# Optimization experiments

Measured on AMD Instinct MI355X. Metric: run time of the kernel, lower is better.

The kernel has to match this reference:

```python
import jax, jax.numpy as jnp
import numpy as np

B, C, D, H, W = 4, 64, 32, 64, 64
S, NH = 8, 4
HD = C // NH


def setup_inputs() -> dict:
    key = jax.random.key(0)
    ks = jax.random.split(key, 8)
    sc = 0.05
    return {
        "x": jax.random.normal(ks[0], (B, C, D, H, W), jnp.float32),
        "slot_init": jax.random.normal(ks[1], (1, C, S), jnp.float32),
        "slot_proj_w": jax.random.normal(ks[2], (C, C), jnp.float32) * sc,
        "slot_proj_b": jnp.zeros((C,), jnp.float32),
        "ln_g": jnp.ones((C,), jnp.float32),
        "ln_b": jnp.zeros((C,), jnp.float32),
        "in_proj_w": jax.random.normal(ks[3], (3 * C, C), jnp.float32) * sc,
        "in_proj_b": jnp.zeros((3 * C,), jnp.float32),
        "out_proj_w": jax.random.normal(ks[4], (C, C), jnp.float32) * sc,
        "out_proj_b": jnp.zeros((C,), jnp.float32),
        "feat_w": jax.random.normal(ks[5], (C, C), jnp.float32) * sc,
        "feat_b": jnp.zeros((C,), jnp.float32),
        "s2f_w": jax.random.normal(ks[6], (C, C), jnp.float32) * sc,
        "s2f_b": jnp.zeros((C,), jnp.float32),
    }


def _l2norm(v, axis):
    # F.normalize: v / max(||v||, eps)
    n = jnp.sqrt(jnp.sum(v * v, axis=axis, keepdims=True))
    return v / jnp.maximum(n, 1e-12)


def reference(x, slot_init, slot_proj_w, slot_proj_b, ln_g, ln_b,
              in_proj_w, in_proj_b, out_proj_w, out_proj_b,
              feat_w, feat_b, s2f_w, s2f_b):
    b, c, d, h, w = x.shape
    n = d * h * w
    x_flat = x.reshape(b, c, n)                                  # (b,c,N)
    slots = jnp.broadcast_to(slot_init, (b, c, S))               # (b,c,S)

    # ---- slot update: cosine-sim cross attention over N ----
    x_norm = _l2norm(x_flat, 1)
    slots_norm = _l2norm(slots, 1)
    sim = jnp.einsum('bcs,bcn->bsn', slots_norm, x_norm)         # (b,S,N)
    attn = jax.nn.softmax(sim, axis=2)
    updates = jnp.einsum('bcn,bsn->bsc', x_flat, attn)           # (b,S,c)
    slots_t = updates @ slot_proj_w.T + slot_proj_b              # (b,S,c)

    # ---- LayerNorm(channels) then tiny MHSA over S=8 slots ----
    mu = jnp.mean(slots_t, axis=-1, keepdims=True)
    var = jnp.mean((slots_t - mu) ** 2, axis=-1, keepdims=True)
    sn = (slots_t - mu) / jnp.sqrt(var + 1e-5) * ln_g + ln_b     # (b,S,c)

    qkv = sn @ in_proj_w.T + in_proj_b                           # (b,S,3c)
    q, k, v = jnp.split(qkv, 3, axis=-1)
    def heads(t):
        return t.reshape(b, S, NH, HD).transpose(0, 2, 1, 3)     # (b,H,S,hd)
    q, k, v = heads(q), heads(k), heads(v)
    scores = jnp.einsum('bhqd,bhkd->bhqk', q, k) / jnp.sqrt(jnp.float32(HD))
    a = jax.nn.softmax(scores, axis=-1)
    o = jnp.einsum('bhqk,bhkd->bhqd', a, v).transpose(0, 2, 1, 3).reshape(b, S, c)
    o = o @ out_proj_w.T + out_proj_b
    slots_t = slots_t + o                                        # (b,S,c)

    # ---- feature broadcast: 1x1x1 conv + slot->feature attention ----
    feat_flat = jnp.einsum('oc,bcn->bon', feat_w, x_flat) + feat_b[None, :, None]
    slots_feat = slots_t @ s2f_w.T + s2f_b                       # (b,S,c)
    sim2 = jnp.einsum('bsc,bcn->bsn', slots_feat, feat_flat)
    attn2 = jax.nn.softmax(sim2, axis=1)                         # softmax over slots
    out = jnp.einsum('bsc,bsn->bcn', slots_t, attn2)             # (b,c,N)
    return out.reshape(b, c, d, h, w) + x
```

## Files before the change

### kernel.cpp

```cpp
#include <hip/hip_runtime.h>
#include <hip/hip_bf16.h>

#define BB   4
#define CC   64
#define SS   8
#define NN   (32*64*64)
#define NH_  4
#define HD_  16
#define TN   256

typedef __attribute__((ext_vector_type(8))) short bf16x8;
typedef __attribute__((ext_vector_type(4))) float f32x4;

__device__ __forceinline__ float b2f(unsigned short h) {
    union { unsigned u; float f; } v; v.u = ((unsigned)h) << 16; return v.f;
}
__device__ __forceinline__ unsigned short f2b(float f) {
    union { float f; unsigned u; } v; v.f = f;
    unsigned r = v.u + 0x7FFFu + ((v.u >> 16) & 1u);
    return (unsigned short)(r >> 16);
}
__device__ __forceinline__ unsigned bfpack(float a, float b) {
    union { float f; unsigned u; } x, y; x.f = a; y.f = b;
    unsigned ra = (x.u + 0x7FFFu + ((x.u >> 16) & 1u)) >> 16;
    unsigned rb = (y.u + 0x7FFFu + ((y.u >> 16) & 1u)) & 0xFFFF0000u;
    return ra | rb;
}

__global__ __launch_bounds__(256) void k_slots_attn(
    const float* __restrict__ x, const float* __restrict__ slot_init,
    float* __restrict__ U_part, float* __restrict__ sume_part, int bpb)
{
    __shared__ short xt[CC * TN];
    __shared__ short et[16 * TN];
    __shared__ float snT[SS * CC];
    __shared__ float snorm[SS];
    __shared__ float red[SS * 256];

    const int tid = threadIdx.x;
    const int b   = blockIdx.x / bpb;
    const int blk = blockIdx.x % bpb;

    *(int4*)&et[8*TN + tid*8] = make_int4(0, 0, 0, 0);

    if (tid < SS) {
        float ss = 0.f;
        for (int c = 0; c < CC; ++c) { float v = slot_init[c*SS + tid]; ss += v*v; }
        snorm[tid] = fmaxf(sqrtf(ss), 1e-12f);
    }
    __syncthreads();
    if (tid < CC) {
        for (int s = 0; s < SS; ++s) snT[s*CC + tid] = slot_init[tid*SS + s] / snorm[s];
    }
    __syncthreads();

    const int lane = tid & 63, wv = tid >> 6;
    const int cS = tid >> 2, nq = tid & 3;
    f32x4 accU = {0.f, 0.f, 0.f, 0.f};
    float accS[SS];
    #pragma unroll
    for (int s = 0; s < SS; ++s) accS[s] = 0.f;

    const float* xb = x + (size_t)b * CC * NN;
    const int ntiles = NN / TN;

    for (int t = blk; t < ntiles; t += bpb) {
        const int n0 = t * TN;

        {
            const float* srcrow = xb + (size_t)cS * NN + n0;
            #pragma unroll
            for (int i = 0; i < 8; ++i) {
                const int n = nq*8 + i*32;
                float4 va = *(const float4*)(srcrow + n);
                float4 vb = *(const float4*)(srcrow + n + 4);
                int4 o;
                o.x = (int)bfpack(va.x, va.y);
                o.y = (int)bfpack(va.z, va.w);
                o.z = (int)bfpack(vb.x, vb.y);
                o.w = (int)bfpack(vb.z, vb.w);
                const int slot = (nq + i*4) ^ (cS & 7);
                *(int4*)&xt[cS*TN + (slot << 3)] = o;
            }
        }
        __syncthreads();

        {
            const int nq3 = tid >> 3, n7 = tid & 7;
            float ss = 0.f;
            float a[SS];
            #pragma unroll
            for (int s = 0; s < SS; ++s) a[s] = 0.f;
            #pragma unroll
            for (int c4 = 0; c4 < 16; ++c4) {
                float xv[4];
                #pragma unroll
                for (int j = 0; j < 4; ++j) {
                    const int c = c4*4 + j;
                    unsigned short h = (unsigned short)xt[c*TN + (((nq3 ^ (c & 7)) << 3) | n7)];
                    xv[j] = b2f(h);
                    ss += xv[j] * xv[j];
                }
                #pragma unroll
                for (int s = 0; s < SS; ++s) {
                    const float4 g4 = *(const float4*)&snT[s*CC + c4*4];
                    a[s] += g4.x*xv[0] + g4.y*xv[1] + g4.z*xv[2] + g4.w*xv[3];
                }
            }
            const float invn = 1.f / fmaxf(sqrtf(ss), 1e-12f);
            #pragma unroll
            for (int s = 0; s < SS; ++s) {
                float e = __expf(a[s] * invn);
                accS[s] += e;
                et[s*TN + (((nq3 ^ s) << 3) | n7)] = (short)f2b(e);
            }
        }
        __syncthreads();

        {
            const int ca = (wv << 4) + (lane & 15);
            const int rb = lane & 15;
            const int p  = lane >> 4;
            #pragma unroll
            for (int k = 0; k < TN/32; ++k) {
                const int sa = ((((k << 2) + p) ^ (lane & 7)) << 3);
                bf16x8 af = *(const bf16x8*)&xt[ca*TN + sa];
                bf16x8 bfr = *(const bf16x8*)&et[rb*TN + sa];
                accU = __builtin_amdgcn_mfma_f32_16x16x32_bf16(af, bfr, accU, 0, 0, 0);
            }
        }
        __syncthreads();
    }

    {
        const size_t base = ((size_t)(b*bpb + blk) * SS) * CC;
        if ((lane & 15) < SS) {
            const int s  = lane & 15;
            const int c0 = (wv << 4) + ((lane >> 4) << 2);
            #pragma unroll
            for (int r = 0; r < 4; ++r)
                U_part[base + s*CC + c0 + r] = accU[r];
        }
    }
    #pragma unroll
    for (int s = 0; s < SS; ++s) red[s*256 + tid] = accS[s];
    __syncthreads();
    {
        const int s = tid >> 5, j = tid & 31;
        float v = 0.f;
        #pragma unroll
        for (int k = 0; k < 8; ++k) v += red[s*256 + j*8 + k];
        v += __shfl_xor(v, 1); v += __shfl_xor(v, 2); v += __shfl_xor(v, 4);
        v += __shfl_xor(v, 8); v += __shfl_xor(v, 16);
        if (j == 0) sume_part[(size_t)(b*bpb + blk)*SS + s] = v;
    }
}

__global__ __launch_bounds__(256) void k_precomp(
    const float* __restrict__ s2fw, const float* __restrict__ s2fb,
    const float* __restrict__ fw, const float* __restrict__ fb,
    float* __restrict__ M, float* __restrict__ g0v,
    float* __restrict__ hv, float* __restrict__ h0)
{
    const int tid = threadIdx.x;
    if (blockIdx.x < 16) {
        const int cp = blockIdx.x*4 + (tid >> 6);
        const int c  = tid & 63;
        float acc = 0.f;
        #pragma unroll 8
        for (int o = 0; o < CC; ++o)
            acc += s2fw[o*CC + cp] * fw[o*CC + c];
        M[cp*CC + c] = acc;
    } else {
        if (tid < 64) {
            float acc = 0.f;
            #pragma unroll 8
            for (int o = 0; o < CC; ++o) acc += s2fb[o] * fw[o*CC + tid];
            g0v[tid] = acc;
        } else if (tid < 128) {
            const int cp = tid - 64;
            float acc = 0.f;
            #pragma unroll 8
            for (int o = 0; o < CC; ++o) acc += s2fw[o*CC + cp] * fb[o];
            hv[cp] = acc;
        } else if (tid == 128) {
            float acc = 0.f;
            for (int o = 0; o < CC; ++o) acc += s2fb[o] * fb[o];
            *h0 = acc;
        }
    }
}

__global__ __launch_bounds__(256) void k_reduce2(
    const float* __restrict__ U_part, const float* __restrict__ sume_part,
    float* __restrict__ upd_g, int bpb)
{
    __shared__ float part[4][64];
    __shared__ float lbuf[256];
    __shared__ float Lsh;
    const int tid = threadIdx.x;
    const int b = blockIdx.x >> 3, s = blockIdx.x & 7;
    const int c = tid & 63, kc = tid >> 6;
    const int cnt = bpb >> 2;

    lbuf[tid] = (tid < bpb) ? sume_part[(size_t)(b*bpb + tid)*SS + s] : 0.f;

    float acc = 0.f;
    const float* base = U_part + ((size_t)(b*bpb + kc*cnt)*SS + s)*CC + c;
    for (int k = 0; k < cnt; ++k)
        acc += base[(size_t)k * SS * CC];
    part[kc][c] = acc;
    __syncthreads();

    if (tid < 128) lbuf[tid] += lbuf[tid + 128];
    __syncthreads();
    if (tid < 64) {
        float v = lbuf[tid] + lbuf[tid + 64];
        v += __shfl_xor(v, 1); v += __shfl_xor(v, 2); v += __shfl_xor(v, 4);
        v += __shfl_xor(v, 8); v += __shfl_xor(v, 16); v += __shfl_xor(v, 32);
        if (tid == 0) Lsh = v;
    }
    __syncthreads();

    if (tid < 64) {
        float u = part[0][c] + part[1][c] + part[2][c] + part[3][c];
        upd_g[((size_t)b*SS + s)*CC + c] = u / Lsh;
    }
}

__global__ __launch_bounds__(256) void k_slots_small(
    const float* __restrict__ upd_g,
    const float* __restrict__ spw, const float* __restrict__ spb,
    const float* __restrict__ lng, const float* __restrict__ lnb,
    const float* __restrict__ ipw, const float* __restrict__ ipb,
    const float* __restrict__ opw, const float* __restrict__ opb,
    const float* __restrict__ M, const float* __restrict__ g0v,
    const float* __restrict__ hv, const float* __restrict__ h0,
    float* __restrict__ st_out, float* __restrict__ g_out, float* __restrict__ h_out)
{
    __shared__ float upd[SS*CC];
    __shared__ float st [SS*CC];
    __shared__ float snb[SS*CC];
    __shared__ float qkv[SS*3*CC];
    __shared__ float ot [SS*CC];

    const int tid  = threadIdx.x;
    const int b    = blockIdx.x;
    const int c    = tid & 63;
    const int quad = tid >> 6;
    const int r0 = quad*2, r1 = r0 + 1;
    float wreg[CC];

    #pragma unroll
    for (int i = 0; i < 16; ++i)
        *(float4*)&wreg[i*4] = *(const float4*)(spw + c*CC + i*4);
    upd[r0*CC + c] = upd_g[(b*SS + r0)*CC + c];
    upd[r1*CC + c] = upd_g[(b*SS + r1)*CC + c];
    __syncthreads();

    {
        const float bias = spb[c];
        float a0 = bias, a1 = bias;
        #pragma unroll
        for (int i = 0; i < 16; ++i) {
            float4 u0 = *(const float4*)&upd[r0*CC + i*4];
            float4 u1 = *(const float4*)&upd[r1*CC + i*4];
            a0 += u0.x*wreg[i*4+0] + u0.y*wreg[i*4+1] + u0.z*wreg[i*4+2] + u0.w*wreg[i*4+3];
            a1 += u1.x*wreg[i*4+0] + u1.y*wreg[i*4+1] + u1.z*wreg[i*4+2] + u1.w*wreg[i*4+3];
        }
        st[r0*CC + c] = a0;
        st[r1*CC + c] = a1;
    }
    __syncthreads();

    {
        const int row = tid >> 5, l = tid & 31;
        float v0 = st[row*CC + l], v1 = st[row*CC + l + 32];
        float sum = v0 + v1;
        sum += __shfl_xor(sum, 1); sum += __shfl_xor(sum, 2); sum += __shfl_xor(sum, 4);
        sum += __shfl_xor(sum, 8); sum += __shfl_xor(sum, 16);
        const float mu = sum * (1.f/64.f);
        const float d0 = v0 - mu, d1 = v1 - mu;
        float vs = d0*d0 + d1*d1;
        vs += __shfl_xor(vs, 1); vs += __shfl_xor(vs, 2); vs += __shfl_xor(vs, 4);
        vs += __shfl_xor(vs, 8); vs += __shfl_xor(vs, 16);
        const float rstd = rsqrtf(vs * (1.f/64.f) + 1e-5f);
        snb[row*CC + l]      = d0 * rstd * lng[l]      + lnb[l];
        snb[row*CC + l + 32] = d1 * rstd * lng[l + 32] + lnb[l + 32];
    }
    __syncthreads();

    for (int m = 0; m < 3; ++m) {
        #pragma unroll
        for (int i = 0; i < 16; ++i)
            *(float4*)&wreg[i*4] = *(const float4*)(ipw + (size_t)(m*CC + c)*CC + i*4);
        const float bias = ipb[m*CC + c];
        float a0 = bias, a1 = bias;
        #pragma unroll
        for (int i = 0; i < 16; ++i) {
            float4 u0 = *(const float4*)&snb[r0*CC + i*4];
            float4 u1 = *(const float4*)&snb[r1*CC + i*4];
            a0 += u0.x*wreg[i*4+0] + u0.y*wreg[i*4+1] + u0.z*wreg[i*4+2] + u0.w*wreg[i*4+3];
            a1 += u1.x*wreg[i*4+0] + u1.y*wreg[i*4+1] + u1.z*wreg[i*4+2] + u1.w*wreg[i*4+3];
        }
        qkv[r0*3*CC + m*CC + c] = a0;
        qkv[r1*3*CC + m*CC + c] = a1;
    }
    __syncthreads();

    if (tid < NH_*SS) {
        const int h = tid >> 3, q = tid & 7;
        float qreg[HD_];
        #pragma unroll
        for (int i = 0; i < 4; ++i)
            *(float4*)&qreg[i*4] = *(const float4*)&qkv[q*3*CC + h*HD_ + i*4];
        float srow[SS];
        float mx = -1e30f;
        #pragma unroll
        for (int k = 0; k < SS; ++k) {
            float acc = 0.f;
            #pragma unroll
            for (int d = 0; d < HD_; ++d)
                acc += qreg[d] * qkv[k*3*CC + CC + h*HD_ + d];
            srow[k] = acc * 0.25f;
            mx = fmaxf(mx, srow[k]);
        }
        float l = 0.f;
        #pragma unroll
        for (int k = 0; k < SS; ++k) { srow[k] = __expf(srow[k] - mx); l += srow[k]; }
        const float inv = 1.f / l;
        float oreg[HD_];
        #pragma unroll
        for (int d = 0; d < HD_; ++d) oreg[d] = 0.f;
        #pragma unroll
        for (int k = 0; k < SS; ++k) {
            #pragma unroll
            for (int d = 0; d < HD_; ++d)
                oreg[d] += srow[k] * qkv[k*3*CC + 2*CC + h*HD_ + d];
        }
        #pragma unroll
        for (int d = 0; d < HD_; ++d)
            ot[q*CC + h*HD_ + d] = oreg[d] * inv;
    }
    __syncthreads();

    #pragma unroll
    for (int i = 0; i < 16; ++i)
        *(float4*)&wreg[i*4] = *(const float4*)(opw + c*CC + i*4);
    {
        const float bias = opb[c];
        float a0 = bias, a1 = bias;
        #pragma unroll
        for (int i = 0; i < 16; ++i) {
            float4 u0 = *(const float4*)&ot[r0*CC + i*4];
            float4 u1 = *(const float4*)&ot[r1*CC + i*4];
            a0 += u0.x*wreg[i*4+0] + u0.y*wreg[i*4+1] + u0.z*wreg[i*4+2] + u0.w*wreg[i*4+3];
            a1 += u1.x*wreg[i*4+0] + u1.y*wreg[i*4+1] + u1.z*wreg[i*4+2] + u1.w*wreg[i*4+3];
        }
        st[r0*CC + c] += a0;
        st[r1*CC + c] += a1;
    }
    __syncthreads();

    #pragma unroll 8
    for (int cp = 0; cp < CC; ++cp) wreg[cp] = M[cp*CC + c];
    {
        const float g0 = g0v[c];
        float a0 = g0, a1 = g0;
        #pragma unroll
        for (int i = 0; i < 16; ++i) {
            float4 s0 = *(const float4*)&st[r0*CC + i*4];
            float4 s1 = *(const float4*)&st[r1*CC + i*4];
            a0 += s0.x*wreg[i*4+0] + s0.y*wreg[i*4+1] + s0.z*wreg[i*4+2] + s0.w*wreg[i*4+3];
            a1 += s1.x*wreg[i*4+0] + s1.y*wreg[i*4+1] + s1.z*wreg[i*4+2] + s1.w*wreg[i*4+3];
        }
        g_out[(b*SS + r0)*CC + c] = a0;
        g_out[(b*SS + r1)*CC + c] = a1;
        st_out[(b*SS + r0)*CC + c] = st[r0*CC + c];
        st_out[(b*SS + r1)*CC + c] = st[r1*CC + c];
    }
    {
        const int row = tid >> 5, l = tid & 31;
        float pv = st[row*CC + l]*hv[l] + st[row*CC + l + 32]*hv[l + 32];
        pv += __shfl_xor(pv, 1); pv += __shfl_xor(pv, 2); pv += __shfl_xor(pv, 4);
        pv += __shfl_xor(pv, 8); pv += __shfl_xor(pv, 16);
        if (l == 0) h_out[b*SS + row] = pv + *h0;
    }
}

__global__ __launch_bounds__(256) void k_feat(
    const float* __restrict__ x,
    const float* __restrict__ st_g, const float* __restrict__ g_g,
    const float* __restrict__ h_g,
    float* __restrict__ out)
{
    __shared__ float stS[SS*CC];
    __shared__ float gS [SS*CC];
    __shared__ float hS [SS];

    const int tid = threadIdx.x;
    const int b  = blockIdx.x >> 9;
    const int n  = ((blockIdx.x & 511) << 8) + tid;

    for (int i = tid; i < SS*CC; i += 256) {
        stS[i] = st_g[b*SS*CC + i];
        gS[i]  = g_g [b*SS*CC + i];
    }
    if (tid < SS) hS[tid] = h_g[b*SS + tid];
    __syncthreads();

    const float* xb = x + (size_t)b * CC * NN + n;
    float xc[CC];
    #pragma unroll
    for (int c = 0; c < CC; ++c) xc[c] = xb[(size_t)c * NN];

    float a[SS];
    #pragma unroll
    for (int s = 0; s < SS; ++s) a[s] = hS[s];
    #pragma unroll
    for (int c4 = 0; c4 < CC/4; ++c4) {
        #pragma unroll
        for (int s = 0; s < SS; ++s) {
            float4 g4 = *(const float4*)(&gS[s*CC + c4*4]);
            a[s] += g4.x*xc[c4*4+0] + g4.y*xc[c4*4+1]
                  + g4.z*xc[c4*4+2] + g4.w*xc[c4*4+3];
        }
    }

    float m = a[0];
    #pragma unroll
    for (int s = 1; s < SS; ++s) m = fmaxf(m, a[s]);
    float l = 0.f;
    #pragma unroll
    for (int s = 0; s < SS; ++s) { a[s] = __expf(a[s] - m); l += a[s]; }
    const float inv = 1.f / l;

    float* ob = out + (size_t)b * CC * NN + n;
    #pragma unroll
    for (int c4 = 0; c4 < CC/4; ++c4) {
        float o0 = 0.f, o1 = 0.f, o2 = 0.f, o3 = 0.f;
        #pragma unroll
        for (int s = 0; s < SS; ++s) {
            float4 s4 = *(const float4*)(&stS[s*CC + c4*4]);
            o0 += s4.x * a[s]; o1 += s4.y * a[s];
            o2 += s4.z * a[s]; o3 += s4.w * a[s];
        }
        ob[(size_t)(c4*4+0) * NN] = o0 * inv + xc[c4*4+0];
        ob[(size_t)(c4*4+1) * NN] = o1 * inv + xc[c4*4+1];
        ob[(size_t)(c4*4+2) * NN] = o2 * inv + xc[c4*4+2];
        ob[(size_t)(c4*4+3) * NN] = o3 * inv + xc[c4*4+3];
    }
}

extern "C" void kernel_launch(void* const* d_in, const int* in_sizes, int n_in,
                              void* d_out, int out_size, void* d_ws, size_t ws_size,
                              hipStream_t stream) {
    const float* x         = (const float*)d_in[0];
    const float* slot_init = (const float*)d_in[1];
    const float* spw       = (const float*)d_in[2];
    const float* spb       = (const float*)d_in[3];
    const float* lng       = (const float*)d_in[4];
    const float* lnb       = (const float*)d_in[5];
    const float* ipw       = (const float*)d_in[6];
    const float* ipb       = (const float*)d_in[7];
    const float* opw       = (const float*)d_in[8];
    const float* opb       = (const float*)d_in[9];
    const float* fw        = (const float*)d_in[10];
    const float* fb        = (const float*)d_in[11];
    const float* s2fw      = (const float*)d_in[12];
    const float* s2fb      = (const float*)d_in[13];
    float* out = (float*)d_out;

    int bpb = 192;
    {
        size_t need = ((size_t)BB*bpb*SS*CC + (size_t)BB*bpb*SS
                       + 2048 + 4096 + 64 + 64 + 64 + 2048 + 2048 + 32) * sizeof(float);
        if (need > ws_size) bpb = 128;
    }

    float* w         = (float*)d_ws;
    float* U_part    = w;
    float* sume_part = U_part + (size_t)BB*bpb*SS*CC;
    float* upd_g     = sume_part + (size_t)BB*bpb*SS;
    float* Mm        = upd_g + 2048;
    float* g0v       = Mm + 4096;
    float* hv        = g0v + 64;
    float* h0        = hv + 64;
    float* st_out    = h0 + 64;
    float* g_out     = st_out + 2048;
    float* h_out     = g_out + 2048;

    k_precomp<<<17, 256, 0, stream>>>(s2fw, s2fb, fw, fb, Mm, g0v, hv, h0);
    k_slots_attn<<<BB * bpb, 256, 0, stream>>>(x, slot_init, U_part, sume_part, bpb);
    k_reduce2<<<BB * SS, 256, 0, stream>>>(U_part, sume_part, upd_g, bpb);
    k_slots_small<<<BB, 256, 0, stream>>>(upd_g, spw, spb, lng, lnb,
                                          ipw, ipb, opw, opb, Mm, g0v, hv, h0,
                                          st_out, g_out, h_out);
    k_feat<<<BB * (NN/256), 256, 0, stream>>>(x, st_out, g_out, h_out, out);
}
```

Baseline: 144.1 us.

## Precompute normalized slots, reuse LDS for reduction, batch x loads, raise blocks per batch

Moves the slot-norm computation out of every k_slots_attn block into an extra block of k_precomp, which writes normalized slots to workspace for the attention kernel to copy in. The separate reduction buffer is dropped by reusing the xt tile memory, cutting LDS per block so more blocks can be resident. All 16 global loads per tile are now issued before packing, to raise memory-level parallelism. Blocks per batch rise from 192 to 512, with k_reduce2 updated to loop over partials; this adds more partial results to reduce.

```diff
diff --git a/kernel.cpp b/kernel.cpp
--- a/kernel.cpp
+++ b/kernel.cpp
@@ -27,32 +27,75 @@
     return ra | rb;
 }
 
+__global__ __launch_bounds__(256) void k_precomp(
+    const float* __restrict__ slot_init,
+    const float* __restrict__ s2fw, const float* __restrict__ s2fb,
+    const float* __restrict__ fw, const float* __restrict__ fb,
+    float* __restrict__ M, float* __restrict__ g0v,
+    float* __restrict__ hv, float* __restrict__ h0,
+    float* __restrict__ snT_ws)
+{
+    const int tid = threadIdx.x;
+    if (blockIdx.x < 16) {
+        const int cp = blockIdx.x*4 + (tid >> 6);
+        const int c  = tid & 63;
+        float acc = 0.f;
+        #pragma unroll 8
+        for (int o = 0; o < CC; ++o)
+            acc += s2fw[o*CC + cp] * fw[o*CC + c];
+        M[cp*CC + c] = acc;
+    } else if (blockIdx.x == 16) {
+        if (tid < 64) {
+            float acc = 0.f;
+            #pragma unroll 8
+            for (int o = 0; o < CC; ++o) acc += s2fb[o] * fw[o*CC + tid];
+            g0v[tid] = acc;
+        } else if (tid < 128) {
+            const int cp = tid - 64;
+            float acc = 0.f;
+            #pragma unroll 8
+            for (int o = 0; o < CC; ++o) acc += s2fw[o*CC + cp] * fb[o];
+            hv[cp] = acc;
+        } else if (tid == 128) {
+            float acc = 0.f;
+            for (int o = 0; o < CC; ++o) acc += s2fb[o] * fb[o];
+            *h0 = acc;
+        }
+    } else {
+        __shared__ float nrm[SS];
+        if (tid < 64) {
+            const int s = tid & 7, ch = tid >> 3;
+            float p = 0.f;
+            #pragma unroll
+            for (int j = 0; j < 8; ++j) {
+                float v = slot_init[(ch*8 + j)*SS + s];
+                p += v*v;
+            }
+            p += __shfl_xor(p, 8); p += __shfl_xor(p, 16); p += __shfl_xor(p, 32);
+            if (tid < 8) nrm[s] = fmaxf(sqrtf(p), 1e-12f);
+        }
+        __syncthreads();
+        for (int i = tid; i < SS*CC; i += 256) {
+            const int s = i >> 6, c = i & 63;
+            snT_ws[i] = slot_init[c*SS + s] / nrm[s];
+        }
+    }
+}
+
 __global__ __launch_bounds__(256) void k_slots_attn(
-    const float* __restrict__ x, const float* __restrict__ slot_init,
+    const float* __restrict__ x, const float* __restrict__ snT_ws,
     float* __restrict__ U_part, float* __restrict__ sume_part, int bpb)
 {
     __shared__ short xt[CC * TN];
     __shared__ short et[16 * TN];
     __shared__ float snT[SS * CC];
-    __shared__ float snorm[SS];
-    __shared__ float red[SS * 256];
 
     const int tid = threadIdx.x;
     const int b   = blockIdx.x / bpb;
     const int blk = blockIdx.x % bpb;
 
     *(int4*)&et[8*TN + tid*8] = make_int4(0, 0, 0, 0);
-
-    if (tid < SS) {
-        float ss = 0.f;
-        for (int c = 0; c < CC; ++c) { float v = slot_init[c*SS + tid]; ss += v*v; }
-        snorm[tid] = fmaxf(sqrtf(ss), 1e-12f);
-    }
-    __syncthreads();
-    if (tid < CC) {
-        for (int s = 0; s < SS; ++s) snT[s*CC + tid] = slot_init[tid*SS + s] / snorm[s];
-    }
-    __syncthreads();
+    if (tid < 128) *(float4*)&snT[tid*4] = *(const float4*)&snT_ws[tid*4];
 
     const int lane = tid & 63, wv = tid >> 6;
     const int cS = tid >> 2, nq = tid & 3;
@@ -68,17 +111,20 @@
         const int n0 = t * TN;
 
         {
-            const float* srcrow = xb + (size_t)cS * NN + n0;
+            const float* srcrow = xb + (size_t)cS * NN + n0 + nq*8;
+            float4 va[8], vb[8];
             #pragma unroll
             for (int i = 0; i < 8; ++i) {
-                const int n = nq*8 + i*32;
-                float4 va = *(const float4*)(srcrow + n);
-                float4 vb = *(const float4*)(srcrow + n + 4);
+                va[i] = *(const float4*)(srcrow + i*32);
+                vb[i] = *(const float4*)(srcrow + i*32 + 4);
+            }
+            #pragma unroll
+            for (int i = 0; i < 8; ++i) {
                 int4 o;
-                o.x = (int)bfpack(va.x, va.y);
-                o.y = (int)bfpack(va.z, va.w);
-                o.z = (int)bfpack(vb.x, vb.y);
-                o.w = (int)bfpack(vb.z, vb.w);
+                o.x = (int)bfpack(va[i].x, va[i].y);
+                o.y = (int)bfpack(va[i].z, va[i].w);
+                o.z = (int)bfpack(vb[i].x, vb[i].y);
+                o.w = (int)bfpack(vb[i].z, vb[i].w);
                 const int slot = (nq + i*4) ^ (cS & 7);
                 *(int4*)&xt[cS*TN + (slot << 3)] = o;
             }
@@ -124,7 +170,7 @@
             #pragma unroll
             for (int k = 0; k < TN/32; ++k) {
                 const int sa = ((((k << 2) + p) ^ (lane & 7)) << 3);
-                bf16x8 af = *(const bf16x8*)&xt[ca*TN + sa];
+                bf16x8 af  = *(const bf16x8*)&xt[ca*TN + sa];
                 bf16x8 bfr = *(const bf16x8*)&et[rb*TN + sa];
                 accU = __builtin_amdgcn_mfma_f32_16x16x32_bf16(af, bfr, accU, 0, 0, 0);
             }
@@ -142,10 +188,11 @@
                 U_part[base + s*CC + c0 + r] = accU[r];
         }
     }
-    #pragma unroll
-    for (int s = 0; s < SS; ++s) red[s*256 + tid] = accS[s];
-    __syncthreads();
-    {
+    {
+        float* red = (float*)xt;
+        #pragma unroll
+        for (int s = 0; s < SS; ++s) red[s*256 + tid] = accS[s];
+        __syncthreads();
         const int s = tid >> 5, j = tid & 31;
         float v = 0.f;
         #pragma unroll
@@ -153,41 +200,6 @@
         v += __shfl_xor(v, 1); v += __shfl_xor(v, 2); v += __shfl_xor(v, 4);
         v += __shfl_xor(v, 8); v += __shfl_xor(v, 16);
         if (j == 0) sume_part[(size_t)(b*bpb + blk)*SS + s] = v;
-    }
-}
-
-__global__ __launch_bounds__(256) void k_precomp(
-    const float* __restrict__ s2fw, const float* __restrict__ s2fb,
-    const float* __restrict__ fw, const float* __restrict__ fb,
-    float* __restrict__ M, float* __restrict__ g0v,
-    float* __restrict__ hv, float* __restrict__ h0)
-{
-    const int tid = threadIdx.x;
-    if (blockIdx.x < 16) {
-        const int cp = blockIdx.x*4 + (tid >> 6);
-        const int c  = tid & 63;
-        float acc = 0.f;
-        #pragma unroll 8
-        for (int o = 0; o < CC; ++o)
-            acc += s2fw[o*CC + cp] * fw[o*CC + c];
-        M[cp*CC + c] = acc;
-    } else {
-        if (tid < 64) {
-            float acc = 0.f;
-            #pragma unroll 8
-            for (int o = 0; o < CC; ++o) acc += s2fb[o] * fw[o*CC + tid];
-            g0v[tid] = acc;
-        } else if (tid < 128) {
-            const int cp = tid - 64;
-            float acc = 0.f;
-            #pragma unroll 8
-            for (int o = 0; o < CC; ++o) acc += s2fw[o*CC + cp] * fb[o];
-            hv[cp] = acc;
-        } else if (tid == 128) {
-            float acc = 0.f;
-            for (int o = 0; o < CC; ++o) acc += s2fb[o] * fb[o];
-            *h0 = acc;
-        }
     }
 }
 
@@ -203,7 +215,10 @@
     const int c = tid & 63, kc = tid >> 6;
     const int cnt = bpb >> 2;
 
-    lbuf[tid] = (tid < bpb) ? sume_part[(size_t)(b*bpb + tid)*SS + s] : 0.f;
+    float lv = 0.f;
+    for (int k = tid; k < bpb; k += 256)
+        lv += sume_part[(size_t)(b*bpb + k)*SS + s];
+    lbuf[tid] = lv;
 
     float acc = 0.f;
     const float* base = U_part + ((size_t)(b*bpb + kc*cnt)*SS + s)*CC + c;
@@ -471,10 +486,11 @@
     const float* s2fb      = (const float*)d_in[13];
     float* out = (float*)d_out;
 
-    int bpb = 192;
+    int bpb = 512;
     {
         size_t need = ((size_t)BB*bpb*SS*CC + (size_t)BB*bpb*SS
-                       + 2048 + 4096 + 64 + 64 + 64 + 2048 + 2048 + 32) * sizeof(float);
+                       + 2048 + 4096 + 64 + 64 + 64 + 1024 + 2048 + 2048 + 32)
+                      * sizeof(float);
         if (need > ws_size) bpb = 128;
     }
 
@@ -486,12 +502,14 @@
     float* g0v       = Mm + 4096;
     float* hv        = g0v + 64;
     float* h0        = hv + 64;
-    float* st_out    = h0 + 64;
+    float* snT_ws    = h0 + 64;
+    float* st_out    = snT_ws + 1024;
     float* g_out     = st_out + 2048;
     float* h_out     = g_out + 2048;
 
-    k_precomp<<<17, 256, 0, stream>>>(s2fw, s2fb, fw, fb, Mm, g0v, hv, h0);
-    k_slots_attn<<<BB * bpb, 256, 0, stream>>>(x, slot_init, U_part, sume_part, bpb);
+    k_precomp<<<18, 256, 0, stream>>>(slot_init, s2fw, s2fb, fw, fb,
+                                      Mm, g0v, hv, h0, snT_ws);
+    k_slots_attn<<<BB * bpb, 256, 0, stream>>>(x, snT_ws, U_part, sume_part, bpb);
     k_reduce2<<<BB * SS, 256, 0, stream>>>(U_part, sume_part, upd_g, bpb);
     k_slots_small<<<BB, 256, 0, stream>>>(upd_g, spw, spb, lng, lnb,
                                           ipw, ipb, opw, opb, Mm, g0v, hv, h0,
```

Measured after the change: 167.9 us. 1.17x slower.
